# Kernel optimization log

Measured on AMD Instinct MI355X. Metric: run time of the kernel, lower is better.

## Reference

```python
import jax, jax.numpy as jnp
import numpy as np

STRIDES = (8, 16, 32)
SIZES = ((80, 80), (40, 40), (20, 20))  # 640x640 input
PRE_TOP_K = 1000
KEEP_TOP_K = 100
IOU_THR = 0.65
SCORE_THR = 0.25
CLASS_OFFSET = 4096.0  # > max image extent, for class-aware NMS


def setup_inputs() -> dict:
    key = jax.random.key(0)
    ks = jax.random.split(key, 6)
    B, C = 8, 1203
    d = {}
    for i, (h, w) in enumerate(SIZES):
        d[f"cls_scores_{i}"] = jax.random.normal(ks[i], (B, C, h, w), dtype=jnp.float32)
        d[f"bbox_preds_{i}"] = jax.random.uniform(ks[3 + i], (B, 4, h, w), dtype=jnp.float32)
    return d


def _flatten(feats, ch):
    B = feats[0].shape[0]
    return jnp.concatenate([f.transpose(0, 2, 3, 1).reshape(B, -1, ch) for f in feats], axis=1)


def _priors():
    pts, strs = [], []
    for (h, w), s in zip(SIZES, STRIDES):
        yy, xx = jnp.meshgrid(jnp.arange(h, dtype=jnp.float32), jnp.arange(w, dtype=jnp.float32), indexing="ij")
        pts.append(jnp.stack([(xx.ravel() + 0.5) * s, (yy.ravel() + 0.5) * s], axis=-1))
        strs.append(jnp.full((h * w,), float(s), dtype=jnp.float32))
    return jnp.concatenate(pts, 0), jnp.concatenate(strs, 0)


def _decode(priors, preds, stride):
    # DistancePointBBoxCoder: preds are LTRB distances scaled by stride.
    d = preds * stride[None, :, None]  # [B,N,4]
    x1 = priors[None, :, 0] - d[..., 0]
    y1 = priors[None, :, 1] - d[..., 1]
    x2 = priors[None, :, 0] + d[..., 2]
    y2 = priors[None, :, 1] + d[..., 3]
    return jnp.stack([x1, y1, x2, y2], axis=-1)


def _iou_matrix(b):
    area = (b[:, 2] - b[:, 0]) * (b[:, 3] - b[:, 1])
    lt = jnp.maximum(b[:, None, :2], b[None, :, :2])
    rb = jnp.minimum(b[:, None, 2:], b[None, :, 2:])
    wh = jnp.clip(rb - lt, 0.0)
    inter = wh[..., 0] * wh[..., 1]
    return inter / (area[:, None] + area[None, :] - inter + 1e-7)


def _nms_single(boxes, scores, labels):
    # boxes [N,4], scores [N] (max over classes), labels [N] int
    ts, idx = jax.lax.top_k(scores, PRE_TOP_K)
    b = boxes[idx]
    l = labels[idx]
    valid = ts > SCORE_THR
    off = b + (l.astype(b.dtype) * CLASS_OFFSET)[:, None]  # class-aware trick
    iou = _iou_matrix(off)  # [K,K]

    def body(keep, i):
        suppressed = jnp.any(keep & (iou[:, i] > IOU_THR))
        keep = keep.at[i].set(valid[i] & ~suppressed)
        return keep, None

    keep, _ = jax.lax.scan(body, jnp.zeros((PRE_TOP_K,), bool), jnp.arange(PRE_TOP_K))
    kept_scores = jnp.where(keep, ts, -1.0)
    fs, fi = jax.lax.top_k(kept_scores, KEEP_TOP_K)
    m = fs > 0.0
    det_boxes = jnp.where(m[:, None], b[fi], 0.0)
    det_scores = jnp.where(m, fs, 0.0)
    det_labels = jnp.where(m, l[fi], -1)
    num_dets = m.sum().astype(jnp.int32)
    return num_dets, det_boxes, det_scores, det_labels


def reference(cls_scores_0, cls_scores_1, cls_scores_2, bbox_preds_0, bbox_preds_1, bbox_preds_2):
    C = cls_scores_0.shape[1]
    cls_scores = jax.nn.sigmoid(_flatten([cls_scores_0, cls_scores_1, cls_scores_2], C))  # [B,N,C]
    preds = _flatten([bbox_preds_0, bbox_preds_1, bbox_preds_2], 4)  # [B,N,4]
    priors, stride = _priors()
    boxes = _decode(priors, preds, stride)  # [B,N,4]
    max_scores = cls_scores.max(axis=-1)  # [B,N]
    labels = cls_scores.argmax(axis=-1)  # [B,N]
    num_dets, det_boxes, det_scores, det_labels = jax.vmap(_nms_single)(boxes, max_scores, labels)
    return num_dets, det_boxes, det_scores, det_labels
```

## Files before the change

kernel.cpp:

```cpp
#include <hip/hip_runtime.h>
#include <math.h>

#pragma clang fp contract(off)

typedef unsigned long long u64;
typedef unsigned int u32;
typedef float f4 __attribute__((ext_vector_type(4)));
typedef unsigned long long u64x2 __attribute__((ext_vector_type(2)));

#define BB 8
#define CC_TOT 1203
#define NANC 8400
#define NSEG 8
#define SEGN 1050
#define NSEL 1000
#define NCAND 1024
#define NT 1024
#define NBATCH 128
#define NCHUNK_MAX 16

__device__ __forceinline__ u32 okey32(float v) {
  u32 b = __float_as_uint(v);
  return (b & 0x80000000u) ? ~b : (b | 0x80000000u);
}

__device__ __forceinline__ float unokey32(u32 ok) {
  u32 fb = (ok & 0x80000000u) ? (ok & 0x7FFFFFFFu) : ~ok;
  return __uint_as_float(fb);
}

__global__ __launch_bounds__(256) void kmax(const float* __restrict__ cls0,
                                            const float* __restrict__ cls1,
                                            const float* __restrict__ cls2,
                                            u64* __restrict__ part,
                                            int chunkSz, int nchunk) {
  int bx = blockIdx.x;
  int per = nchunk * BB;
  int tg = bx / per;
  int rem = bx - tg * per;
  int chunk = rem >> 3;
  int b = rem & 7;
  const float* cls; int hw4, aoff, col0;
  if (tg < 7)      { cls = cls0; hw4 = 1600; aoff = 0;    col0 = tg << 8; }
  else if (tg < 9) { cls = cls1; hw4 = 400;  aoff = 6400; col0 = (tg - 7) << 8; }
  else             { cls = cls2; hw4 = 100;  aoff = 8000; col0 = 0; }
  int col = col0 + (int)threadIdx.x;
  if (col >= hw4) return;
  int c0 = chunk * chunkSz;
  int c1 = c0 + chunkSz; if (c1 > CC_TOT) c1 = CC_TOT;

  const f4* base = (const f4*)cls + (size_t)b * CC_TOT * hw4 + col;
  f4 m = (f4){-3.4e38f, -3.4e38f, -3.4e38f, -3.4e38f};
  int ix0 = c0, ix1 = c0, ix2 = c0, ix3 = c0;

#define UPD(v, c)                                   \
  do {                                              \
    if ((v)[0] > m[0]) { m[0] = (v)[0]; ix0 = (c); } \
    if ((v)[1] > m[1]) { m[1] = (v)[1]; ix1 = (c); } \
    if ((v)[2] > m[2]) { m[2] = (v)[2]; ix2 = (c); } \
    if ((v)[3] > m[3]) { m[3] = (v)[3]; ix3 = (c); } \
  } while (0)

  int c = c0;
  for (; c + 8 <= c1; c += 8) {
    const f4* p = base + (size_t)c * hw4;
    f4 v0 = p[0];
    f4 v1 = p[(size_t)1 * hw4];
    f4 v2 = p[(size_t)2 * hw4];
    f4 v3 = p[(size_t)3 * hw4];
    f4 v4 = p[(size_t)4 * hw4];
    f4 v5 = p[(size_t)5 * hw4];
    f4 v6 = p[(size_t)6 * hw4];
    f4 v7 = p[(size_t)7 * hw4];
    UPD(v0, c + 0); UPD(v1, c + 1); UPD(v2, c + 2); UPD(v3, c + 3);
    UPD(v4, c + 4); UPD(v5, c + 5); UPD(v6, c + 6); UPD(v7, c + 7);
  }
  for (; c < c1; ++c) {
    f4 v = base[(size_t)c * hw4];
    UPD(v, c);
  }
#undef UPD

  u64* dst = part + ((size_t)chunk * BB + b) * NANC + aoff + (size_t)col * 4;
  u64x2 s01 = { ((u64)okey32(m[0]) << 32) | (u64)(u32)~(u32)ix0,
                ((u64)okey32(m[1]) << 32) | (u64)(u32)~(u32)ix1 };
  u64x2 s23 = { ((u64)okey32(m[2]) << 32) | (u64)(u32)~(u32)ix2,
                ((u64)okey32(m[3]) << 32) | (u64)(u32)~(u32)ix3 };
  *((u64x2*)dst)     = s01;
  *((u64x2*)dst + 1) = s23;
}

struct DecodeArrays {
  float xo1[NCAND], yo1[NCAND], xo2[NCAND], yo2[NCAND], ar[NCAND];
  float rx1[NCAND], ry1[NCAND], rx2[NCAND], ry2[NCAND], sc[NCAND];
  int lab[NCAND], val[NCAND];
};

__device__ __forceinline__ void hist_addc(u32* hist, u32 digit, int lane) {
  u64 peers = ~0ull;
  for (int bit = 0; bit < 13; ++bit) {
    u64 bal = __ballot((digit >> bit) & 1u);
    peers &= ((digit >> bit) & 1u) ? bal : ~bal;
  }
  int leader = __ffsll((unsigned long long)peers) - 1;
  if (digit < 4096u && lane == leader)
    atomicAdd(&hist[digit], (u32)__popcll((unsigned long long)peers));
}

__device__ __forceinline__ void suffix_pick(u32* hist, u32* waveTot, u32* waveSufExcl,
                                            u64* prefixSh, u32* rankSh, u32* binCntSh,
                                            u64 prefix, u32 rank, int shift,
                                            int tid, int lane, int wv) {
  u32 l0 = hist[4 * tid], l1 = hist[4 * tid + 1], l2 = hist[4 * tid + 2], l3 = hist[4 * tid + 3];
  u32 psum = l0 + l1 + l2 + l3;
  u32 x = psum;
  for (int s = 1; s < 64; s <<= 1) { u32 v = __shfl_down(x, s); if (lane + s < 64) x += v; }
  if (lane == 0) waveTot[wv] = x;
  __syncthreads();
  if (tid < 16) {
    u32 y = waveTot[tid]; u32 z = y;
    for (int s = 1; s < 16; s <<= 1) { u32 v = __shfl_down(z, s); if (tid + s < 16) z += v; }
    waveSufExcl[tid] = z - y;
  }
  __syncthreads();
  u32 S = x + waveSufExcl[wv];
  u32 G3 = S - psum; u32 G2 = G3 + l3; u32 G1 = G2 + l2; u32 G0 = G1 + l1;
  u32 r = rank;
  if      (G3 < r && G3 + l3 >= r) { *prefixSh = prefix | ((u64)(4u * tid + 3) << shift); *rankSh = r - G3; *binCntSh = l3; }
  else if (G2 < r && G2 + l2 >= r) { *prefixSh = prefix | ((u64)(4u * tid + 2) << shift); *rankSh = r - G2; *binCntSh = l2; }
  else if (G1 < r && G1 + l1 >= r) { *prefixSh = prefix | ((u64)(4u * tid + 1) << shift); *rankSh = r - G1; *binCntSh = l1; }
  else if (G0 < r && G0 + l0 >= r) { *prefixSh = prefix | ((u64)(4u * tid + 0) << shift); *rankSh = r - G0; *binCntSh = l0; }
}

__device__ __forceinline__ u64 select_after_hist(const u64* keys, int n, u32 target,
                                                 u32* hist, u32* waveTot, u32* waveSufExcl,
                                                 u64* prefixSh, u32* rankSh, u32* binCntSh,
                                                 int tid, int lane, int wv) {
  suffix_pick(hist, waveTot, waveSufExcl, prefixSh, rankSh, binCntSh,
              0ull, target, 52, tid, lane, wv);
  __syncthreads();
  u64 pfx = *prefixSh; u32 rk = *rankSh; u32 lc = *binCntSh;
  __syncthreads();
  if (lc == rk) return pfx;
  for (int pass = 2; pass >= 0; --pass) {
    int shift = 16 + pass * 12;
    for (int i = tid; i < 4096; i += NT) hist[i] = 0;
    __syncthreads();
    u64 hiMask = (~0ull) << (shift + 12);
    for (int i = tid; i < n; i += NT) {
      u64 k = keys[i];
      if ((k & hiMask) == (pfx & hiMask))
        atomicAdd(&hist[(u32)((k >> shift) & 4095u)], 1u);
    }
    __syncthreads();
    suffix_pick(hist, waveTot, waveSufExcl, prefixSh, rankSh, binCntSh,
                pfx, rk, shift, tid, lane, wv);
    __syncthreads();
    pfx = *prefixSh; rk = *rankSh; lc = *binCntSh;
    __syncthreads();
    if (lc == rk) break;
  }
  return pfx;
}

__device__ __forceinline__ void gather_ge(const u64* keys, int n, u64 K, u64* dst, u32* cnt,
                                          int tid, int lane, u32 bound) {
  for (int i = tid; i < n; i += NT) {
    u64 k = keys[i];
    bool sel = (k >= K);
    u64 mask = __ballot(sel);
    if (mask) {
      int leader = __ffsll((unsigned long long)mask) - 1;
      u32 basep = 0;
      if (lane == leader) basep = atomicAdd(cnt, (u32)__popcll((unsigned long long)mask));
      basep = __shfl((int)basep, leader);
      if (sel) {
        u32 pos = basep + (u32)__popcll((unsigned long long)(mask & ((1ull << lane) - 1ull)));
        if (pos < bound) dst[pos] = k;
      }
    }
  }
}

__global__ __launch_bounds__(1024) void kseg(const u64* __restrict__ part, int nchunk,
                                             u64* __restrict__ candSeg) {
  __shared__ __align__(16) u64 keys[SEGN];
  __shared__ u32 hist[4096];
  __shared__ u32 waveTot[16], waveSufExcl[16];
  __shared__ u64 prefixSh;
  __shared__ u32 rankSh, binCntSh, cnt;

  int seg = blockIdx.x >> 3;
  int b = blockIdx.x & 7;
  int tid = threadIdx.x, lane = tid & 63, wv = tid >> 6;
  int a0 = seg * SEGN;

  const u64x2* psrc = (const u64x2*)part + ((size_t)b * NANC + a0) / 2;
  const size_t PL2 = (size_t)BB * NANC / 2;

  for (int i = tid; i < 4096; i += NT) hist[i] = 0;
  if (tid == 0) cnt = 0;
  __syncthreads();

  {
    u32 d0 = 4096u, d1 = 4096u;
    if (tid < SEGN / 2) {
      u64x2 m = psrc[tid];
      int ch = 1;
      for (; ch + 4 <= nchunk; ch += 4) {
        u64x2 v0 = psrc[(size_t)(ch + 0) * PL2 + tid];
        u64x2 v1 = psrc[(size_t)(ch + 1) * PL2 + tid];
        u64x2 v2 = psrc[(size_t)(ch + 2) * PL2 + tid];
        u64x2 v3 = psrc[(size_t)(ch + 3) * PL2 + tid];
        u64 a01 = (v0[0] > v1[0]) ? v0[0] : v1[0];
        u64 a23 = (v2[0] > v3[0]) ? v2[0] : v3[0];
        u64 aa = (a01 > a23) ? a01 : a23;
        if (aa > m[0]) m[0] = aa;
        u64 b01 = (v0[1] > v1[1]) ? v0[1] : v1[1];
        u64 b23 = (v2[1] > v3[1]) ? v2[1] : v3[1];
        u64 bb2_ = (b01 > b23) ? b01 : b23;
        if (bb2_ > m[1]) m[1] = bb2_;
      }
      for (; ch < nchunk; ++ch) {
        u64x2 v = psrc[(size_t)ch * PL2 + tid];
        if (v[0] > m[0]) m[0] = v[0];
        if (v[1] > m[1]) m[1] = v[1];
      }
      u32 aA = (u32)(a0 + 2 * tid), aB = aA + 1;
      u64 k0 = (m[0] & 0xFFFFFFFF00000000ull) | ((u64)(0xFFFFu - aA) << 16) | (u64)(~(u32)m[0] & 0xFFFFu);
      u64 k1 = (m[1] & 0xFFFFFFFF00000000ull) | ((u64)(0xFFFFu - aB) << 16) | (u64)(~(u32)m[1] & 0xFFFFu);
      keys[2 * tid] = k0;
      keys[2 * tid + 1] = k1;
      d0 = (u32)(k0 >> 52);
      d1 = (u32)(k1 >> 52);
    }
    hist_addc(hist, d0, lane);
    hist_addc(hist, d1, lane);
  }
  __syncthreads();

  u64 K = select_after_hist(keys, SEGN, NBATCH, hist, waveTot, waveSufExcl,
                            &prefixSh, &rankSh, &binCntSh, tid, lane, wv);
  gather_ge(keys, SEGN, K, candSeg + ((size_t)b * NSEG + seg) * NBATCH, &cnt,
            tid, lane, NBATCH);
}

__device__ __forceinline__ void decode_into(DecodeArrays* d, int rk, u64 my, int b,
                                            const float* bb0, const float* bb1, const float* bb2) {
  int label = (int)(u32)(my & 0xFFFFull);
  int idx = 0xFFFF - (int)(u32)((my >> 16) & 0xFFFFull);
  float logit = unokey32((u32)(my >> 32));
  float sc = 1.0f / (1.0f + expf(-logit));

  int w, str, off, hwl; const float* bb;
  if (idx < 6400)      { w = 80; str = 8;  off = 0;    hwl = 6400; bb = bb0; }
  else if (idx < 8000) { w = 40; str = 16; off = 6400; hwl = 1600; bb = bb1; }
  else                 { w = 20; str = 32; off = 8000; hwl = 400;  bb = bb2; }
  int p = idx - off;
  int y = p / w;
  int x = p - y * w;
  float fs = (float)str;
  float px = ((float)x + 0.5f) * fs;
  float py = ((float)y + 0.5f) * fs;
  const float* bp = bb + (size_t)b * 4 * hwl + p;
  float t0 = bp[0] * fs;
  float t1 = bp[hwl] * fs;
  float t2 = bp[2 * hwl] * fs;
  float t3 = bp[3 * hwl] * fs;
  float x1 = px - t0, y1 = py - t1, x2 = px + t2, y2 = py + t3;
  float lo = (float)label * 4096.0f;
  float ox1 = x1 + lo, oy1 = y1 + lo, ox2 = x2 + lo, oy2 = y2 + lo;
  float area = (ox2 - ox1) * (oy2 - oy1);

  d->xo1[rk] = ox1; d->yo1[rk] = oy1; d->xo2[rk] = ox2; d->yo2[rk] = oy2; d->ar[rk] = area;
  d->rx1[rk] = x1;  d->ry1[rk] = y1;  d->rx2[rk] = x2;  d->ry2[rk] = y2;  d->sc[rk] = sc;
  d->lab[rk] = label;
  d->val[rk] = (sc > 0.25f) ? 1 : 0;
}

__device__ __forceinline__ int nms_pass(const DecodeArrays* d, int bound, int lane, int* outIdx) {
  float ax1 = 0, ay1 = 0, ax2 = 0, ay2 = 0, aar = 0; int aon = 0;
  float bx1 = 0, by1 = 0, bx2 = 0, by2 = 0, bar = 0; int bon = 0;
  int kept = 0;
  for (int i = 0; i < bound; ++i) {
    if (kept >= 100) break;
    float cx1 = d->xo1[i], cy1 = d->yo1[i], cx2 = d->xo2[i], cy2 = d->yo2[i], car = d->ar[i];
    bool sup = false;
    if (aon) {
      float ltx = fmaxf(ax1, cx1), lty = fmaxf(ay1, cy1);
      float rbx = fminf(ax2, cx2), rby = fminf(ay2, cy2);
      float wd = fmaxf(rbx - ltx, 0.0f), ht = fmaxf(rby - lty, 0.0f);
      float inter = wd * ht;
      sup = sup || ((inter / (aar + car - inter + 1e-7f)) > 0.65f);
    }
    if (bon) {
      float ltx = fmaxf(bx1, cx1), lty = fmaxf(by1, cy1);
      float rbx = fminf(bx2, cx2), rby = fminf(by2, cy2);
      float wd = fmaxf(rbx - ltx, 0.0f), ht = fmaxf(rby - lty, 0.0f);
      float inter = wd * ht;
      sup = sup || ((inter / (bar + car - inter + 1e-7f)) > 0.65f);
    }
    bool anysup = __any(sup);
    if (d->val[i] != 0 && !anysup) {
      if (kept < 64) {
        if (lane == kept) { ax1 = cx1; ay1 = cy1; ax2 = cx2; ay2 = cy2; aar = car; aon = 1; }
      } else {
        if (lane == kept - 64) { bx1 = cx1; by1 = cy1; bx2 = cx2; by2 = cy2; bar = car; bon = 1; }
      }
      if (lane == 0) outIdx[kept] = i;
      ++kept;
    }
  }
  return kept;
}

__global__ __launch_bounds__(1024) void kmerge(const u64* __restrict__ part, int nchunk,
                                               const u64* __restrict__ candSeg,
                                               const float* __restrict__ bb0,
                                               const float* __restrict__ bb1,
                                               const float* __restrict__ bb2,
                                               float* __restrict__ out) {
  __shared__ union ShU {
    u64 fk[NANC];
    DecodeArrays d;
  } sh;
  __shared__ u32 hist[4096];
  __shared__ u32 waveTot[16], waveSufExcl[16];
  __shared__ u64 prefixSh;
  __shared__ u32 rankSh, binCntSh;
  __shared__ u32 gcnt, aCnt;
  __shared__ __align__(16) u64 cand[NCAND];
  __shared__ __align__(16) u64 candA[NBATCH];
  __shared__ __align__(16) u32 cm[NBATCH * 4];
  __shared__ u64 VwSh[2];
  __shared__ int outIdx[128];
  __shared__ int keptSh;

  int b = blockIdx.x;
  int tid = threadIdx.x;
  int lane = tid & 63;
  int wv = tid >> 6;

  for (int i = tid; i < 4096; i += NT) hist[i] = 0;
  if (tid == 0) { gcnt = 0; aCnt = 0; }
  __syncthreads();
  u64 myk = candSeg[(size_t)b * (NSEG * NBATCH) + tid];
  cand[tid] = myk;
  hist_addc(hist, (u32)(myk >> 52), lane);
  if (tid < NBATCH * 4) cm[tid] = 0;
  __syncthreads();

  u64 K = select_after_hist(cand, NCAND, NBATCH, hist, waveTot, waveSufExcl,
                            &prefixSh, &rankSh, &binCntSh, tid, lane, wv);
  gather_ge(cand, NCAND, K, candA, &aCnt, tid, lane, NBATCH);
  __syncthreads();

  if (tid < NBATCH) {
    u64 my = candA[tid];
    int rk = 0;
    const u64x2* cav = (const u64x2*)candA;
    #pragma unroll
    for (int j2 = 0; j2 < NBATCH / 2; ++j2) {
      u64x2 p = cav[j2];
      rk += (p[0] > my) ? 1 : 0;
      rk += (p[1] > my) ? 1 : 0;
    }
    decode_into(&sh.d, rk, my, b, bb0, bb1, bb2);
  }
  __syncthreads();

  if (tid < NBATCH) {
    u64 bal = __ballot(sh.d.val[tid] != 0);
    if (lane == 0) VwSh[tid >> 6] = bal;
  }

  {
    int c = tid & 127;
    int g = tid >> 7;
    float cx1 = sh.d.xo1[c], cy1 = sh.d.yo1[c], cx2 = sh.d.xo2[c], cy2 = sh.d.yo2[c], car = sh.d.ar[c];
    u32 bits = 0;
    int j0 = g * 16;
    for (int jj = 0; jj < 16; ++jj) {
      int j = j0 + jj;
      float ltx = fmaxf(sh.d.xo1[j], cx1), lty = fmaxf(sh.d.yo1[j], cy1);
      float rbx = fminf(sh.d.xo2[j], cx2), rby = fminf(sh.d.yo2[j], cy2);
      float wd = fmaxf(rbx - ltx, 0.0f), ht = fmaxf(rby - lty, 0.0f);
      float inter = wd * ht;
      bool sup = (inter / (sh.d.ar[j] + car - inter + 1e-7f)) > 0.65f;
      bits |= sup ? (1u << jj) : 0u;
    }
    atomicOr(&cm[c * 4 + (g >> 1)], bits << ((g & 1) * 16));
  }
  __syncthreads();

  if (tid == 0) {
    u32 L0 = (u32)VwSh[0], L1 = (u32)(VwSh[0] >> 32);
    u32 L2 = (u32)VwSh[1], L3 = (u32)(VwSh[1] >> 32);
    int kept = 0;
    while (kept < 100) {
      int i;
      if (L0)      i = __ffs(L0) - 1;
      else if (L1) i = 31 + __ffs(L1);
      else if (L2) i = 63 + __ffs(L2);
      else if (L3) i = 95 + __ffs(L3);
      else break;
      outIdx[kept++] = i;
      const u32* c4 = &cm[i * 4];
      L0 &= ~c4[0]; L1 &= ~c4[1]; L2 &= ~c4[2]; L3 &= ~c4[3];
      if (i < 32)      L0 &= ~(1u << i);
      else if (i < 64) L1 &= ~(1u << (i - 32));
      else if (i < 96) L2 &= ~(1u << (i - 64));
      else             L3 &= ~(1u << (i - 96));
    }
    keptSh = kept;
  }
  __syncthreads();

  if (keptSh < 100) {
    const u64x2* psrc = (const u64x2*)(part + (size_t)b * NANC);
    const size_t PL2 = (size_t)BB * NANC / 2;
    for (int i = tid; i < 4096; i += NT) hist[i] = 0;
    __syncthreads();
    {
      u64x2* fdst = (u64x2*)sh.fk;
      for (int i = tid; i < NANC / 2; i += NT) {
        u64x2 m = psrc[i];
        for (int ch = 1; ch < nchunk; ++ch) {
          u64x2 v = psrc[(size_t)ch * PL2 + i];
          if (v[0] > m[0]) m[0] = v[0];
          if (v[1] > m[1]) m[1] = v[1];
        }
        u32 i0 = (u32)(2 * i), i1 = (u32)(2 * i + 1);
        u64x2 r;
        r[0] = (m[0] & 0xFFFFFFFF00000000ull) | ((u64)(0xFFFFu - i0) << 16) | (u64)(~(u32)m[0] & 0xFFFFu);
        r[1] = (m[1] & 0xFFFFFFFF00000000ull) | ((u64)(0xFFFFu - i1) << 16) | (u64)(~(u32)m[1] & 0xFFFFu);
        fdst[i] = r;
        hist_addc(hist, (u32)(r[0] >> 52), lane);
        hist_addc(hist, (u32)(r[1] >> 52), lane);
      }
    }
    __syncthreads();
    u64 Kf = select_after_hist(sh.fk, NANC, NSEL, hist, waveTot, waveSufExcl,
                               &prefixSh, &rankSh, &binCntSh, tid, lane, wv);
    gather_ge(sh.fk, NANC, Kf, cand, &gcnt, tid, lane, NSEL);
    __syncthreads();
    if (tid < NSEL) {
      u64 my = cand[tid];
      int rk = 0;
      const u64x2* cbv = (const u64x2*)cand;
      for (int j2 = 0; j2 < NSEL / 2; ++j2) {
        u64x2 p = cbv[j2];
        rk += (p[0] > my) ? 1 : 0;
        rk += (p[1] > my) ? 1 : 0;
      }
      decode_into(&sh.d, rk, my, b, bb0, bb1, bb2);
    }
    __syncthreads();
    if (tid < 64) {
      int kept = nms_pass(&sh.d, NSEL, lane, outIdx);
      if (lane == 0) keptSh = kept;
    }
    __syncthreads();
  }

  int kept = keptSh;
  float* o_nd = out;
  float* o_box = out + BB;
  float* o_sc = out + BB + BB * 100 * 4;
  float* o_lb = out + BB + BB * 100 * 4 + BB * 100;
  if (tid == 0) o_nd[b] = (float)kept;
  if (tid < 100) {
    int s = tid;
    float v0 = 0, v1 = 0, v2 = 0, v3 = 0, sv = 0, lv = -1.0f;
    if (s < kept) {
      int i = outIdx[s];
      v0 = sh.d.rx1[i]; v1 = sh.d.ry1[i]; v2 = sh.d.rx2[i]; v3 = sh.d.ry2[i];
      sv = sh.d.sc[i]; lv = (float)sh.d.lab[i];
    }
    float* bo = o_box + ((size_t)b * 100 + s) * 4;
    bo[0] = v0; bo[1] = v1; bo[2] = v2; bo[3] = v3;
    o_sc[b * 100 + s] = sv;
    o_lb[b * 100 + s] = lv;
  }
}

extern "C" void kernel_launch(void* const* d_in, const int* in_sizes, int n_in,
                              void* d_out, int out_size, void* d_ws, size_t ws_size,
                              hipStream_t stream) {
  const float* cls0 = (const float*)d_in[0];
  const float* bb0  = (const float*)d_in[1];
  const float* cls1 = (const float*)d_in[2];
  const float* bb1  = (const float*)d_in[3];
  const float* cls2 = (const float*)d_in[4];
  const float* bb2  = (const float*)d_in[5];

  size_t planeB = (size_t)BB * NANC * sizeof(u64);
  size_t candB = (size_t)BB * NSEG * NBATCH * sizeof(u64);
  u64* part = (u64*)d_ws;
  int nchunk = 1;
  if (ws_size > candB + planeB) {
    nchunk = (int)((ws_size - candB) / planeB);
    if (nchunk > NCHUNK_MAX) nchunk = NCHUNK_MAX;
    if (nchunk < 1) nchunk = 1;
  }
  int chunkSz = (CC_TOT + nchunk - 1) / nchunk;
  nchunk = (CC_TOT + chunkSz - 1) / chunkSz;
  u64* candSeg = part + (size_t)nchunk * BB * NANC;

  kmax<<<dim3(10 * nchunk * BB), dim3(256), 0, stream>>>(cls0, cls1, cls2, part, chunkSz, nchunk);
  kseg<<<dim3(NSEG * BB), dim3(NT), 0, stream>>>(part, nchunk, candSeg);
  kmerge<<<dim3(BB), dim3(NT), 0, stream>>>(part, nchunk, candSeg, bb0, bb1, bb2, (float*)d_out);
}
```

Before: 119.8 us.

## Fuse max, segment-select and merge kernels into one cooperative kernel

Merges the three kernel launches (per-chunk class max, per-segment top-k selection, per-image merge/NMS) into a single cooperative kernel that uses grid-wide syncs between phases. Each 1024-thread block runs four 256-thread virtual tiles of the former max kernel, and the chunk cap drops from 16 to 12 so the grid fits co-resident. The aim is to remove launch gaps and per-kernel tails. The costs are fewer, larger blocks in the bandwidth-heavy max phase, a large shared-memory footprint limiting occupancy during that phase, and the overhead of grid.sync.

```diff
diff --git a/kernel.cpp b/kernel.cpp
--- a/kernel.cpp
+++ b/kernel.cpp
@@ -1,7 +1,10 @@
 #include <hip/hip_runtime.h>
+#include <hip/hip_cooperative_groups.h>
 #include <math.h>
 
 #pragma clang fp contract(off)
+
+namespace cg = cooperative_groups;
 
 typedef unsigned long long u64;
 typedef unsigned int u32;
@@ -17,7 +20,7 @@
 #define NCAND 1024
 #define NT 1024
 #define NBATCH 128
-#define NCHUNK_MAX 16
+#define NCHUNK_MAX 12
 
 __device__ __forceinline__ u32 okey32(float v) {
   u32 b = __float_as_uint(v);
@@ -27,67 +30,6 @@
 __device__ __forceinline__ float unokey32(u32 ok) {
   u32 fb = (ok & 0x80000000u) ? (ok & 0x7FFFFFFFu) : ~ok;
   return __uint_as_float(fb);
-}
-
-__global__ __launch_bounds__(256) void kmax(const float* __restrict__ cls0,
-                                            const float* __restrict__ cls1,
-                                            const float* __restrict__ cls2,
-                                            u64* __restrict__ part,
-                                            int chunkSz, int nchunk) {
-  int bx = blockIdx.x;
-  int per = nchunk * BB;
-  int tg = bx / per;
-  int rem = bx - tg * per;
-  int chunk = rem >> 3;
-  int b = rem & 7;
-  const float* cls; int hw4, aoff, col0;
-  if (tg < 7)      { cls = cls0; hw4 = 1600; aoff = 0;    col0 = tg << 8; }
-  else if (tg < 9) { cls = cls1; hw4 = 400;  aoff = 6400; col0 = (tg - 7) << 8; }
-  else             { cls = cls2; hw4 = 100;  aoff = 8000; col0 = 0; }
-  int col = col0 + (int)threadIdx.x;
-  if (col >= hw4) return;
-  int c0 = chunk * chunkSz;
-  int c1 = c0 + chunkSz; if (c1 > CC_TOT) c1 = CC_TOT;
-
-  const f4* base = (const f4*)cls + (size_t)b * CC_TOT * hw4 + col;
-  f4 m = (f4){-3.4e38f, -3.4e38f, -3.4e38f, -3.4e38f};
-  int ix0 = c0, ix1 = c0, ix2 = c0, ix3 = c0;
-
-#define UPD(v, c)                                   \
-  do {                                              \
-    if ((v)[0] > m[0]) { m[0] = (v)[0]; ix0 = (c); } \
-    if ((v)[1] > m[1]) { m[1] = (v)[1]; ix1 = (c); } \
-    if ((v)[2] > m[2]) { m[2] = (v)[2]; ix2 = (c); } \
-    if ((v)[3] > m[3]) { m[3] = (v)[3]; ix3 = (c); } \
-  } while (0)
-
-  int c = c0;
-  for (; c + 8 <= c1; c += 8) {
-    const f4* p = base + (size_t)c * hw4;
-    f4 v0 = p[0];
-    f4 v1 = p[(size_t)1 * hw4];
-    f4 v2 = p[(size_t)2 * hw4];
-    f4 v3 = p[(size_t)3 * hw4];
-    f4 v4 = p[(size_t)4 * hw4];
-    f4 v5 = p[(size_t)5 * hw4];
-    f4 v6 = p[(size_t)6 * hw4];
-    f4 v7 = p[(size_t)7 * hw4];
-    UPD(v0, c + 0); UPD(v1, c + 1); UPD(v2, c + 2); UPD(v3, c + 3);
-    UPD(v4, c + 4); UPD(v5, c + 5); UPD(v6, c + 6); UPD(v7, c + 7);
-  }
-  for (; c < c1; ++c) {
-    f4 v = base[(size_t)c * hw4];
-    UPD(v, c);
-  }
-#undef UPD
-
-  u64* dst = part + ((size_t)chunk * BB + b) * NANC + aoff + (size_t)col * 4;
-  u64x2 s01 = { ((u64)okey32(m[0]) << 32) | (u64)(u32)~(u32)ix0,
-                ((u64)okey32(m[1]) << 32) | (u64)(u32)~(u32)ix1 };
-  u64x2 s23 = { ((u64)okey32(m[2]) << 32) | (u64)(u32)~(u32)ix2,
-                ((u64)okey32(m[3]) << 32) | (u64)(u32)~(u32)ix3 };
-  *((u64x2*)dst)     = s01;
-  *((u64x2*)dst + 1) = s23;
 }
 
 struct DecodeArrays {
@@ -180,69 +122,6 @@
       }
     }
   }
-}
-
-__global__ __launch_bounds__(1024) void kseg(const u64* __restrict__ part, int nchunk,
-                                             u64* __restrict__ candSeg) {
-  __shared__ __align__(16) u64 keys[SEGN];
-  __shared__ u32 hist[4096];
-  __shared__ u32 waveTot[16], waveSufExcl[16];
-  __shared__ u64 prefixSh;
-  __shared__ u32 rankSh, binCntSh, cnt;
-
-  int seg = blockIdx.x >> 3;
-  int b = blockIdx.x & 7;
-  int tid = threadIdx.x, lane = tid & 63, wv = tid >> 6;
-  int a0 = seg * SEGN;
-
-  const u64x2* psrc = (const u64x2*)part + ((size_t)b * NANC + a0) / 2;
-  const size_t PL2 = (size_t)BB * NANC / 2;
-
-  for (int i = tid; i < 4096; i += NT) hist[i] = 0;
-  if (tid == 0) cnt = 0;
-  __syncthreads();
-
-  {
-    u32 d0 = 4096u, d1 = 4096u;
-    if (tid < SEGN / 2) {
-      u64x2 m = psrc[tid];
-      int ch = 1;
-      for (; ch + 4 <= nchunk; ch += 4) {
-        u64x2 v0 = psrc[(size_t)(ch + 0) * PL2 + tid];
-        u64x2 v1 = psrc[(size_t)(ch + 1) * PL2 + tid];
-        u64x2 v2 = psrc[(size_t)(ch + 2) * PL2 + tid];
-        u64x2 v3 = psrc[(size_t)(ch + 3) * PL2 + tid];
-        u64 a01 = (v0[0] > v1[0]) ? v0[0] : v1[0];
-        u64 a23 = (v2[0] > v3[0]) ? v2[0] : v3[0];
-        u64 aa = (a01 > a23) ? a01 : a23;
-        if (aa > m[0]) m[0] = aa;
-        u64 b01 = (v0[1] > v1[1]) ? v0[1] : v1[1];
-        u64 b23 = (v2[1] > v3[1]) ? v2[1] : v3[1];
-        u64 bb2_ = (b01 > b23) ? b01 : b23;
-        if (bb2_ > m[1]) m[1] = bb2_;
-      }
-      for (; ch < nchunk; ++ch) {
-        u64x2 v = psrc[(size_t)ch * PL2 + tid];
-        if (v[0] > m[0]) m[0] = v[0];
-        if (v[1] > m[1]) m[1] = v[1];
-      }
-      u32 aA = (u32)(a0 + 2 * tid), aB = aA + 1;
-      u64 k0 = (m[0] & 0xFFFFFFFF00000000ull) | ((u64)(0xFFFFu - aA) << 16) | (u64)(~(u32)m[0] & 0xFFFFu);
-      u64 k1 = (m[1] & 0xFFFFFFFF00000000ull) | ((u64)(0xFFFFu - aB) << 16) | (u64)(~(u32)m[1] & 0xFFFFu);
-      keys[2 * tid] = k0;
-      keys[2 * tid + 1] = k1;
-      d0 = (u32)(k0 >> 52);
-      d1 = (u32)(k1 >> 52);
-    }
-    hist_addc(hist, d0, lane);
-    hist_addc(hist, d1, lane);
-  }
-  __syncthreads();
-
-  u64 K = select_after_hist(keys, SEGN, NBATCH, hist, waveTot, waveSufExcl,
-                            &prefixSh, &rankSh, &binCntSh, tid, lane, wv);
-  gather_ge(keys, SEGN, K, candSeg + ((size_t)b * NSEG + seg) * NBATCH, &cnt,
-            tid, lane, NBATCH);
 }
 
 __device__ __forceinline__ void decode_into(DecodeArrays* d, int rk, u64 my, int b,
@@ -314,12 +193,16 @@
   return kept;
 }
 
-__global__ __launch_bounds__(1024) void kmerge(const u64* __restrict__ part, int nchunk,
-                                               const u64* __restrict__ candSeg,
-                                               const float* __restrict__ bb0,
-                                               const float* __restrict__ bb1,
-                                               const float* __restrict__ bb2,
-                                               float* __restrict__ out) {
+__global__ __launch_bounds__(1024) void kall(const float* __restrict__ cls0,
+                                             const float* __restrict__ cls1,
+                                             const float* __restrict__ cls2,
+                                             const float* __restrict__ bb0,
+                                             const float* __restrict__ bb1,
+                                             const float* __restrict__ bb2,
+                                             u64* __restrict__ part,
+                                             u64* __restrict__ candSeg,
+                                             float* __restrict__ out,
+                                             int chunkSz, int nchunk, int ntiles) {
   __shared__ union ShU {
     u64 fk[NANC];
     DecodeArrays d;
@@ -336,151 +219,277 @@
   __shared__ int outIdx[128];
   __shared__ int keptSh;
 
-  int b = blockIdx.x;
+  cg::grid_group grid = cg::this_grid();
   int tid = threadIdx.x;
   int lane = tid & 63;
   int wv = tid >> 6;
 
-  for (int i = tid; i < 4096; i += NT) hist[i] = 0;
-  if (tid == 0) { gcnt = 0; aCnt = 0; }
-  __syncthreads();
-  u64 myk = candSeg[(size_t)b * (NSEG * NBATCH) + tid];
-  cand[tid] = myk;
-  hist_addc(hist, (u32)(myk >> 52), lane);
-  if (tid < NBATCH * 4) cm[tid] = 0;
-  __syncthreads();
-
-  u64 K = select_after_hist(cand, NCAND, NBATCH, hist, waveTot, waveSufExcl,
-                            &prefixSh, &rankSh, &binCntSh, tid, lane, wv);
-  gather_ge(cand, NCAND, K, candA, &aCnt, tid, lane, NBATCH);
-  __syncthreads();
-
-  if (tid < NBATCH) {
-    u64 my = candA[tid];
-    int rk = 0;
-    const u64x2* cav = (const u64x2*)candA;
-    #pragma unroll
-    for (int j2 = 0; j2 < NBATCH / 2; ++j2) {
-      u64x2 p = cav[j2];
-      rk += (p[0] > my) ? 1 : 0;
-      rk += (p[1] > my) ? 1 : 0;
-    }
-    decode_into(&sh.d, rk, my, b, bb0, bb1, bb2);
-  }
-  __syncthreads();
-
-  if (tid < NBATCH) {
-    u64 bal = __ballot(sh.d.val[tid] != 0);
-    if (lane == 0) VwSh[tid >> 6] = bal;
-  }
-
   {
-    int c = tid & 127;
-    int g = tid >> 7;
-    float cx1 = sh.d.xo1[c], cy1 = sh.d.yo1[c], cx2 = sh.d.xo2[c], cy2 = sh.d.yo2[c], car = sh.d.ar[c];
-    u32 bits = 0;
-    int j0 = g * 16;
-    for (int jj = 0; jj < 16; ++jj) {
-      int j = j0 + jj;
-      float ltx = fmaxf(sh.d.xo1[j], cx1), lty = fmaxf(sh.d.yo1[j], cy1);
-      float rbx = fminf(sh.d.xo2[j], cx2), rby = fminf(sh.d.yo2[j], cy2);
-      float wd = fmaxf(rbx - ltx, 0.0f), ht = fmaxf(rby - lty, 0.0f);
-      float inter = wd * ht;
-      bool sup = (inter / (sh.d.ar[j] + car - inter + 1e-7f)) > 0.65f;
-      bits |= sup ? (1u << jj) : 0u;
-    }
-    atomicOr(&cm[c * 4 + (g >> 1)], bits << ((g & 1) * 16));
-  }
-  __syncthreads();
-
-  if (tid == 0) {
-    u32 L0 = (u32)VwSh[0], L1 = (u32)(VwSh[0] >> 32);
-    u32 L2 = (u32)VwSh[1], L3 = (u32)(VwSh[1] >> 32);
-    int kept = 0;
-    while (kept < 100) {
-      int i;
-      if (L0)      i = __ffs(L0) - 1;
-      else if (L1) i = 31 + __ffs(L1);
-      else if (L2) i = 63 + __ffs(L2);
-      else if (L3) i = 95 + __ffs(L3);
-      else break;
-      outIdx[kept++] = i;
-      const u32* c4 = &cm[i * 4];
-      L0 &= ~c4[0]; L1 &= ~c4[1]; L2 &= ~c4[2]; L3 &= ~c4[3];
-      if (i < 32)      L0 &= ~(1u << i);
-      else if (i < 64) L1 &= ~(1u << (i - 32));
-      else if (i < 96) L2 &= ~(1u << (i - 64));
-      else             L3 &= ~(1u << (i - 96));
-    }
-    keptSh = kept;
-  }
-  __syncthreads();
-
-  if (keptSh < 100) {
-    const u64x2* psrc = (const u64x2*)(part + (size_t)b * NANC);
+    int sub = tid >> 8;
+    int t = tid & 255;
+    int vt = blockIdx.x * 4 + sub;
+    if (vt < ntiles) {
+      int per = nchunk * BB;
+      int tg = vt / per;
+      int rem = vt - tg * per;
+      int chunk = rem >> 3;
+      int b = rem & 7;
+      const float* cls; int hw4, aoff, col0;
+      if (tg < 7)      { cls = cls0; hw4 = 1600; aoff = 0;    col0 = tg << 8; }
+      else if (tg < 9) { cls = cls1; hw4 = 400;  aoff = 6400; col0 = (tg - 7) << 8; }
+      else             { cls = cls2; hw4 = 100;  aoff = 8000; col0 = 0; }
+      int col = col0 + t;
+      if (col < hw4) {
+        int c0 = chunk * chunkSz;
+        int c1 = c0 + chunkSz; if (c1 > CC_TOT) c1 = CC_TOT;
+        const f4* base = (const f4*)cls + (size_t)b * CC_TOT * hw4 + col;
+        f4 m = (f4){-3.4e38f, -3.4e38f, -3.4e38f, -3.4e38f};
+        int ix0 = c0, ix1 = c0, ix2 = c0, ix3 = c0;
+
+#define UPD(v, c)                                   \
+  do {                                              \
+    if ((v)[0] > m[0]) { m[0] = (v)[0]; ix0 = (c); } \
+    if ((v)[1] > m[1]) { m[1] = (v)[1]; ix1 = (c); } \
+    if ((v)[2] > m[2]) { m[2] = (v)[2]; ix2 = (c); } \
+    if ((v)[3] > m[3]) { m[3] = (v)[3]; ix3 = (c); } \
+  } while (0)
+
+        int c = c0;
+        for (; c + 8 <= c1; c += 8) {
+          const f4* p = base + (size_t)c * hw4;
+          f4 v0 = p[0];
+          f4 v1 = p[(size_t)1 * hw4];
+          f4 v2 = p[(size_t)2 * hw4];
+          f4 v3 = p[(size_t)3 * hw4];
+          f4 v4 = p[(size_t)4 * hw4];
+          f4 v5 = p[(size_t)5 * hw4];
+          f4 v6 = p[(size_t)6 * hw4];
+          f4 v7 = p[(size_t)7 * hw4];
+          UPD(v0, c + 0); UPD(v1, c + 1); UPD(v2, c + 2); UPD(v3, c + 3);
+          UPD(v4, c + 4); UPD(v5, c + 5); UPD(v6, c + 6); UPD(v7, c + 7);
+        }
+        for (; c < c1; ++c) {
+          f4 v = base[(size_t)c * hw4];
+          UPD(v, c);
+        }
+#undef UPD
+
+        u64* dst = part + ((size_t)chunk * BB + b) * NANC + aoff + (size_t)col * 4;
+        u64x2 s01 = { ((u64)okey32(m[0]) << 32) | (u64)(u32)~(u32)ix0,
+                      ((u64)okey32(m[1]) << 32) | (u64)(u32)~(u32)ix1 };
+        u64x2 s23 = { ((u64)okey32(m[2]) << 32) | (u64)(u32)~(u32)ix2,
+                      ((u64)okey32(m[3]) << 32) | (u64)(u32)~(u32)ix3 };
+        *((u64x2*)dst)     = s01;
+        *((u64x2*)dst + 1) = s23;
+      }
+    }
+  }
+  __threadfence();
+  grid.sync();
+
+  if (blockIdx.x < NSEG * BB) {
+    int seg = blockIdx.x >> 3;
+    int b = blockIdx.x & 7;
+    int a0 = seg * SEGN;
+    u64* keys = sh.fk;
+
+    const u64x2* psrc = (const u64x2*)part + ((size_t)b * NANC + a0) / 2;
     const size_t PL2 = (size_t)BB * NANC / 2;
+
     for (int i = tid; i < 4096; i += NT) hist[i] = 0;
-    __syncthreads();
+    if (tid == 0) aCnt = 0;
+    __syncthreads();
+
     {
-      u64x2* fdst = (u64x2*)sh.fk;
-      for (int i = tid; i < NANC / 2; i += NT) {
-        u64x2 m = psrc[i];
-        for (int ch = 1; ch < nchunk; ++ch) {
-          u64x2 v = psrc[(size_t)ch * PL2 + i];
+      u32 d0 = 4096u, d1 = 4096u;
+      if (tid < SEGN / 2) {
+        u64x2 m = psrc[tid];
+        int ch = 1;
+        for (; ch + 4 <= nchunk; ch += 4) {
+          u64x2 v0 = psrc[(size_t)(ch + 0) * PL2 + tid];
+          u64x2 v1 = psrc[(size_t)(ch + 1) * PL2 + tid];
+          u64x2 v2 = psrc[(size_t)(ch + 2) * PL2 + tid];
+          u64x2 v3 = psrc[(size_t)(ch + 3) * PL2 + tid];
+          u64 a01 = (v0[0] > v1[0]) ? v0[0] : v1[0];
+          u64 a23 = (v2[0] > v3[0]) ? v2[0] : v3[0];
+          u64 aa = (a01 > a23) ? a01 : a23;
+          if (aa > m[0]) m[0] = aa;
+          u64 b01 = (v0[1] > v1[1]) ? v0[1] : v1[1];
+          u64 b23 = (v2[1] > v3[1]) ? v2[1] : v3[1];
+          u64 bb2_ = (b01 > b23) ? b01 : b23;
+          if (bb2_ > m[1]) m[1] = bb2_;
+        }
+        for (; ch < nchunk; ++ch) {
+          u64x2 v = psrc[(size_t)ch * PL2 + tid];
           if (v[0] > m[0]) m[0] = v[0];
           if (v[1] > m[1]) m[1] = v[1];
         }
-        u32 i0 = (u32)(2 * i), i1 = (u32)(2 * i + 1);
-        u64x2 r;
-        r[0] = (m[0] & 0xFFFFFFFF00000000ull) | ((u64)(0xFFFFu - i0) << 16) | (u64)(~(u32)m[0] & 0xFFFFu);
-        r[1] = (m[1] & 0xFFFFFFFF00000000ull) | ((u64)(0xFFFFu - i1) << 16) | (u64)(~(u32)m[1] & 0xFFFFu);
-        fdst[i] = r;
-        hist_addc(hist, (u32)(r[0] >> 52), lane);
-        hist_addc(hist, (u32)(r[1] >> 52), lane);
-      }
-    }
-    __syncthreads();
-    u64 Kf = select_after_hist(sh.fk, NANC, NSEL, hist, waveTot, waveSufExcl,
-                               &prefixSh, &rankSh, &binCntSh, tid, lane, wv);
-    gather_ge(sh.fk, NANC, Kf, cand, &gcnt, tid, lane, NSEL);
-    __syncthreads();
-    if (tid < NSEL) {
-      u64 my = cand[tid];
+        u32 aA = (u32)(a0 + 2 * tid), aB = aA + 1;
+        u64 k0 = (m[0] & 0xFFFFFFFF00000000ull) | ((u64)(0xFFFFu - aA) << 16) | (u64)(~(u32)m[0] & 0xFFFFu);
+        u64 k1 = (m[1] & 0xFFFFFFFF00000000ull) | ((u64)(0xFFFFu - aB) << 16) | (u64)(~(u32)m[1] & 0xFFFFu);
+        keys[2 * tid] = k0;
+        keys[2 * tid + 1] = k1;
+        d0 = (u32)(k0 >> 52);
+        d1 = (u32)(k1 >> 52);
+      }
+      hist_addc(hist, d0, lane);
+      hist_addc(hist, d1, lane);
+    }
+    __syncthreads();
+
+    u64 K = select_after_hist(keys, SEGN, NBATCH, hist, waveTot, waveSufExcl,
+                              &prefixSh, &rankSh, &binCntSh, tid, lane, wv);
+    gather_ge(keys, SEGN, K, candSeg + ((size_t)b * NSEG + seg) * NBATCH, &aCnt,
+              tid, lane, NBATCH);
+  }
+  __threadfence();
+  grid.sync();
+
+  if (blockIdx.x >= BB) return;
+  {
+    int b = blockIdx.x;
+
+    for (int i = tid; i < 4096; i += NT) hist[i] = 0;
+    if (tid == 0) { gcnt = 0; aCnt = 0; }
+    __syncthreads();
+    u64 myk = candSeg[(size_t)b * (NSEG * NBATCH) + tid];
+    cand[tid] = myk;
+    hist_addc(hist, (u32)(myk >> 52), lane);
+    if (tid < NBATCH * 4) cm[tid] = 0;
+    __syncthreads();
+
+    u64 K = select_after_hist(cand, NCAND, NBATCH, hist, waveTot, waveSufExcl,
+                              &prefixSh, &rankSh, &binCntSh, tid, lane, wv);
+    gather_ge(cand, NCAND, K, candA, &aCnt, tid, lane, NBATCH);
+    __syncthreads();
+
+    if (tid < NBATCH) {
+      u64 my = candA[tid];
       int rk = 0;
-      const u64x2* cbv = (const u64x2*)cand;
-      for (int j2 = 0; j2 < NSEL / 2; ++j2) {
-        u64x2 p = cbv[j2];
+      const u64x2* cav = (const u64x2*)candA;
+      #pragma unroll
+      for (int j2 = 0; j2 < NBATCH / 2; ++j2) {
+        u64x2 p = cav[j2];
         rk += (p[0] > my) ? 1 : 0;
         rk += (p[1] > my) ? 1 : 0;
       }
       decode_into(&sh.d, rk, my, b, bb0, bb1, bb2);
     }
     __syncthreads();
-    if (tid < 64) {
-      int kept = nms_pass(&sh.d, NSEL, lane, outIdx);
-      if (lane == 0) keptSh = kept;
-    }
-    __syncthreads();
-  }
-
-  int kept = keptSh;
-  float* o_nd = out;
-  float* o_box = out + BB;
-  float* o_sc = out + BB + BB * 100 * 4;
-  float* o_lb = out + BB + BB * 100 * 4 + BB * 100;
-  if (tid == 0) o_nd[b] = (float)kept;
-  if (tid < 100) {
-    int s = tid;
-    float v0 = 0, v1 = 0, v2 = 0, v3 = 0, sv = 0, lv = -1.0f;
-    if (s < kept) {
-      int i = outIdx[s];
-      v0 = sh.d.rx1[i]; v1 = sh.d.ry1[i]; v2 = sh.d.rx2[i]; v3 = sh.d.ry2[i];
-      sv = sh.d.sc[i]; lv = (float)sh.d.lab[i];
-    }
-    float* bo = o_box + ((size_t)b * 100 + s) * 4;
-    bo[0] = v0; bo[1] = v1; bo[2] = v2; bo[3] = v3;
-    o_sc[b * 100 + s] = sv;
-    o_lb[b * 100 + s] = lv;
+
+    if (tid < NBATCH) {
+      u64 bal = __ballot(sh.d.val[tid] != 0);
+      if (lane == 0) VwSh[tid >> 6] = bal;
+    }
+
+    {
+      int c = tid & 127;
+      int g = tid >> 7;
+      float cx1 = sh.d.xo1[c], cy1 = sh.d.yo1[c], cx2 = sh.d.xo2[c], cy2 = sh.d.yo2[c], car = sh.d.ar[c];
+      u32 bits = 0;
+      int j0 = g * 16;
+      for (int jj = 0; jj < 16; ++jj) {
+        int j = j0 + jj;
+        float ltx = fmaxf(sh.d.xo1[j], cx1), lty = fmaxf(sh.d.yo1[j], cy1);
+        float rbx = fminf(sh.d.xo2[j], cx2), rby = fminf(sh.d.yo2[j], cy2);
+        float wd = fmaxf(rbx - ltx, 0.0f), ht = fmaxf(rby - lty, 0.0f);
+        float inter = wd * ht;
+        bool sup = (inter / (sh.d.ar[j] + car - inter + 1e-7f)) > 0.65f;
+        bits |= sup ? (1u << jj) : 0u;
+      }
+      atomicOr(&cm[c * 4 + (g >> 1)], bits << ((g & 1) * 16));
+    }
+    __syncthreads();
+
+    if (tid == 0) {
+      u32 L0 = (u32)VwSh[0], L1 = (u32)(VwSh[0] >> 32);
+      u32 L2 = (u32)VwSh[1], L3 = (u32)(VwSh[1] >> 32);
+      int kept = 0;
+      while (kept < 100) {
+        int i;
+        if (L0)      i = __ffs(L0) - 1;
+        else if (L1) i = 31 + __ffs(L1);
+        else if (L2) i = 63 + __ffs(L2);
+        else if (L3) i = 95 + __ffs(L3);
+        else break;
+        outIdx[kept++] = i;
+        const u32* c4 = &cm[i * 4];
+        L0 &= ~c4[0]; L1 &= ~c4[1]; L2 &= ~c4[2]; L3 &= ~c4[3];
+        if (i < 32)      L0 &= ~(1u << i);
+        else if (i < 64) L1 &= ~(1u << (i - 32));
+        else if (i < 96) L2 &= ~(1u << (i - 64));
+        else             L3 &= ~(1u << (i - 96));
+      }
+      keptSh = kept;
+    }
+    __syncthreads();
+
+    if (keptSh < 100) {
+      const u64x2* psrc = (const u64x2*)(part + (size_t)b * NANC);
+      const size_t PL2 = (size_t)BB * NANC / 2;
+      for (int i = tid; i < 4096; i += NT) hist[i] = 0;
+      __syncthreads();
+      {
+        u64x2* fdst = (u64x2*)sh.fk;
+        for (int i = tid; i < NANC / 2; i += NT) {
+          u64x2 m = psrc[i];
+          for (int ch = 1; ch < nchunk; ++ch) {
+            u64x2 v = psrc[(size_t)ch * PL2 + i];
+            if (v[0] > m[0]) m[0] = v[0];
+            if (v[1] > m[1]) m[1] = v[1];
+          }
+          u32 i0 = (u32)(2 * i), i1 = (u32)(2 * i + 1);
+          u64x2 r;
+          r[0] = (m[0] & 0xFFFFFFFF00000000ull) | ((u64)(0xFFFFu - i0) << 16) | (u64)(~(u32)m[0] & 0xFFFFu);
+          r[1] = (m[1] & 0xFFFFFFFF00000000ull) | ((u64)(0xFFFFu - i1) << 16) | (u64)(~(u32)m[1] & 0xFFFFu);
+          fdst[i] = r;
+          hist_addc(hist, (u32)(r[0] >> 52), lane);
+          hist_addc(hist, (u32)(r[1] >> 52), lane);
+        }
+      }
+      __syncthreads();
+      u64 Kf = select_after_hist(sh.fk, NANC, NSEL, hist, waveTot, waveSufExcl,
+                                 &prefixSh, &rankSh, &binCntSh, tid, lane, wv);
+      gather_ge(sh.fk, NANC, Kf, cand, &gcnt, tid, lane, NSEL);
+      __syncthreads();
+      if (tid < NSEL) {
+        u64 my = cand[tid];
+        int rk = 0;
+        const u64x2* cbv = (const u64x2*)cand;
+        for (int j2 = 0; j2 < NSEL / 2; ++j2) {
+          u64x2 p = cbv[j2];
+          rk += (p[0] > my) ? 1 : 0;
+          rk += (p[1] > my) ? 1 : 0;
+        }
+        decode_into(&sh.d, rk, my, b, bb0, bb1, bb2);
+      }
+      __syncthreads();
+      if (tid < 64) {
+        int kept = nms_pass(&sh.d, NSEL, lane, outIdx);
+        if (lane == 0) keptSh = kept;
+      }
+      __syncthreads();
+    }
+
+    int kept = keptSh;
+    float* o_nd = out;
+    float* o_box = out + BB;
+    float* o_sc = out + BB + BB * 100 * 4;
+    float* o_lb = out + BB + BB * 100 * 4 + BB * 100;
+    if (tid == 0) o_nd[b] = (float)kept;
+    if (tid < 100) {
+      int s = tid;
+      float v0 = 0, v1 = 0, v2 = 0, v3 = 0, sv = 0, lv = -1.0f;
+      if (s < kept) {
+        int i = outIdx[s];
+        v0 = sh.d.rx1[i]; v1 = sh.d.ry1[i]; v2 = sh.d.rx2[i]; v3 = sh.d.ry2[i];
+        sv = sh.d.sc[i]; lv = (float)sh.d.lab[i];
+      }
+      float* bo = o_box + ((size_t)b * 100 + s) * 4;
+      bo[0] = v0; bo[1] = v1; bo[2] = v2; bo[3] = v3;
+      o_sc[b * 100 + s] = sv;
+      o_lb[b * 100 + s] = lv;
+    }
   }
 }
 
@@ -507,7 +516,13 @@
   nchunk = (CC_TOT + chunkSz - 1) / chunkSz;
   u64* candSeg = part + (size_t)nchunk * BB * NANC;
 
-  kmax<<<dim3(10 * nchunk * BB), dim3(256), 0, stream>>>(cls0, cls1, cls2, part, chunkSz, nchunk);
-  kseg<<<dim3(NSEG * BB), dim3(NT), 0, stream>>>(part, nchunk, candSeg);
-  kmerge<<<dim3(BB), dim3(NT), 0, stream>>>(part, nchunk, candSeg, bb0, bb1, bb2, (float*)d_out);
-}
+  int ntiles = 10 * nchunk * BB;
+  int nb = (ntiles + 3) / 4;
+  if (nb < NSEG * BB) nb = NSEG * BB;
+
+  void* args[] = { (void*)&cls0, (void*)&cls1, (void*)&cls2,
+                   (void*)&bb0,  (void*)&bb1,  (void*)&bb2,
+                   (void*)&part, (void*)&candSeg, (void*)&d_out,
+                   (void*)&chunkSz, (void*)&nchunk, (void*)&ntiles };
+  hipLaunchCooperativeKernel((void*)kall, dim3(nb), dim3(NT), args, 0, stream);
+}
```

Measured after the change: 423.8 us. 254% more time.
